# Kernel tuning notes

Measured on AMD Instinct MI355X. Metric: run time of the kernel, lower is better.

Reference implementation:

```python
import jax, jax.numpy as jnp
import numpy as np

PIXEL_THRESHOLD = 0.4
FRACTION_THRESHOLD = 0.03
NUM_CLASSES = 20
N, H, W = 100, 640, 960
LOGIT_SCALE = 8.0  # makes the instance-axis softmax peaky enough to cross PIXEL_THRESHOLD


def setup_inputs() -> dict:
    key = jax.random.key(0)
    k1, k2, k3 = jax.random.split(key, 3)
    cls_prob = jax.random.uniform(k1, (N,), dtype=jnp.float32)
    mask_prob = jax.random.normal(k2, (N, H, W), dtype=jnp.float32) * LOGIT_SCALE
    cls_idx = jax.random.randint(k3, (N,), 0, NUM_CLASSES)
    return {"cls_prob": cls_prob, "mask_prob": mask_prob, "cls_idx": cls_idx}


def _mask_removal(cls_prob, mask_prob, cls_idx):
    # Sort instances by class confidence, descending (greedy NMS order).
    order = jnp.argsort(-cls_prob)
    cls_prob_s = cls_prob[order]          # [N]
    cls_idx_s = cls_idx[order]            # [N]
    raw_s = mask_prob[order]              # [N,H,W] pre-softmax logits (mask_prob_copy)
    # Per-pixel softmax over the instance axis (permutation-equivariant, so
    # softmax-then-sort == sort-then-softmax as in the original).
    sm = jax.nn.softmax(raw_s, axis=0)    # [N,H,W]

    def step(state, inp):
        panoptic, mask_image = state      # [H,W], [C,H,W]
        smi, rawi, ci = inp
        logit = (smi >= PIXEL_THRESHOLD).astype(rawi.dtype)   # binarized mask [H,W]
        mask_sum = logit.sum()
        curr = mask_image[ci]
        overlap = jnp.sum((curr >= 1.0) & (logit == 1.0)).astype(rawi.dtype) / jnp.maximum(mask_sum, 1.0)
        degenerate = (logit.max() == logit.min()) | (mask_sum == 0.0)
        skip = degenerate | (overlap > FRACTION_THRESHOLD)
        # assign only unclaimed panoptic pixels inside the binarized mask
        assign = (panoptic == 0.0) & (logit == 1.0) & jnp.logical_not(skip)
        keep_mask = jnp.where(assign, rawi, 0.0)              # use_mask_low_constant=False
        panoptic = jnp.where(assign, 1.0, panoptic)
        mask_image = mask_image.at[ci].add(jnp.where(assign, logit, 0.0))
        return (panoptic, mask_image), (keep_mask, jnp.logical_not(skip))

    init = (jnp.zeros((H, W), jnp.float32), jnp.zeros((NUM_CLASSES, H, W), jnp.float32))
    _, (keep_masks, keep_flags) = jax.lax.scan(step, init, (sm, raw_s, cls_idx_s))
    # Fixed-shape outputs: keep_flags marks which (sorted) instances survived;
    # dropped instances have all-zero keep_masks rows.
    return cls_prob_s, keep_masks, cls_idx_s, keep_flags


def reference(cls_prob, mask_prob, cls_idx):
    return _mask_removal(cls_prob, mask_prob, cls_idx)
```

## Files before the change

### kernel.cpp

```cpp
#include <hip/hip_runtime.h>
#include <cstdint>
#include <cstddef>

#define N_INST 100
#define HW (640 * 960)
#define PIX_THR 0.4f
#define FRAC_THR 0.03f

#define OUT_MASKS_OFF 100
#define OUT_CLSIDX_OFF (100 + (size_t)N_INST * HW)
#define OUT_FLAGS_OFF (100 + (size_t)N_INST * HW + N_INST)


__global__ void k0_sort(const float* __restrict__ cls_prob,
                        const int* __restrict__ cls_idx,
                        int* __restrict__ ord,
                        float* __restrict__ out) {
    int i = threadIdx.x;
    if (i >= N_INST) return;
    float pi = cls_prob[i];
    int rank = 0;
    for (int j = 0; j < N_INST; ++j) {
        float pj = cls_prob[j];
        rank += (pj > pi) || (pj == pi && j < i);
    }
    ord[rank] = i;
    out[rank] = pi;
    out[OUT_CLSIDX_OFF + rank] = (float)cls_idx[i];
}

__global__ __launch_bounds__(256) void k1_softmax(
    const float* __restrict__ mask,
    const int* __restrict__ ord,
    unsigned* __restrict__ mask_sum,
    unsigned* __restrict__ pair_cnt,
    unsigned* __restrict__ code) {
    __shared__ int sord[N_INST];
    __shared__ unsigned ssum[N_INST];
    int t = threadIdx.x;
    if (t < N_INST) {
        sord[t] = ord[t];
        ssum[t] = 0u;
    }
    __syncthreads();

    int p = blockIdx.x * 256 + t;

    float v[N_INST];
#pragma unroll
    for (int i = 0; i < N_INST; ++i)
        v[i] = mask[(size_t)sord[i] * HW + p];

    float m = v[0];
    int p1 = 0;
    float m2 = -3.4e38f;
    int p2 = 0;
#pragma unroll
    for (int i = 1; i < N_INST; ++i) {
        if (v[i] > m) { m2 = m; p2 = p1; m = v[i]; p1 = i; }
        else if (v[i] > m2) { m2 = v[i]; p2 = i; }
    }

    float d = 0.0f;
#pragma unroll
    for (int i = 0; i < N_INST; ++i)
        d += expf(v[i] - m);

    float sm1 = 1.0f / d;
    float sm2 = expf(m2 - m) / d;
    bool q1 = (sm1 >= PIX_THR);
    bool q2 = (sm2 >= PIX_THR);

    unsigned c = 0u;
    if (q1) {
        atomicAdd(&ssum[p1], 1u);
        if (q2) {
            atomicAdd(&ssum[p2], 1u);
            int a = min(p1, p2);
            int b = max(p1, p2);
            atomicAdd(&pair_cnt[a * N_INST + b], 1u);
            c = (unsigned)(a + 1) | ((unsigned)(b + 1) << 8);
        } else {
            c = (unsigned)(p1 + 1);
        }
    }
    code[p] = c;

    __syncthreads();
    if (t < N_INST && ssum[t] != 0u)
        atomicAdd(&mask_sum[t], ssum[t]);
}

__global__ void k2_scan(const unsigned* __restrict__ mask_sum,
                        const unsigned* __restrict__ pair_cnt,
                        const int* __restrict__ ord,
                        const int* __restrict__ cls_idx,
                        int* __restrict__ keep,
                        float* __restrict__ out) {
    __shared__ unsigned spair[N_INST * N_INST];
    __shared__ int scls[N_INST];
    __shared__ unsigned sms[N_INST];
    __shared__ int skeep[N_INST];
    int t = threadIdx.x;
    for (int i = t; i < N_INST * N_INST; i += 256)
        spair[i] = pair_cnt[i];
    if (t < N_INST) {
        scls[t] = cls_idx[ord[t]];
        sms[t] = mask_sum[t];
    }
    __syncthreads();

    for (int b = 0; b < N_INST; ++b) {
        if (t < 64) {
            unsigned cnt = 0u;
            for (int a = t; a < b; a += 64)
                if (skeep[a] && scls[a] == scls[b])
                    cnt += spair[a * N_INST + b];
#pragma unroll
            for (int off = 32; off; off >>= 1)
                cnt += __shfl_down((int)cnt, off);
            if (t == 0) {
                unsigned ms = sms[b];
                float overlap = (float)cnt / fmaxf((float)ms, 1.0f);
                bool degen = (ms == 0u) || (ms == (unsigned)HW);
                bool skip = degen || (overlap > FRAC_THR);
                skeep[b] = skip ? 0 : 1;
            }
        }
        __syncthreads();
    }

    if (t < N_INST) {
        keep[t] = skeep[t];
        out[OUT_FLAGS_OFF + t] = (float)skeep[t];
    }
}

__global__ __launch_bounds__(256) void k3_write(
    const float* __restrict__ mask,
    const int* __restrict__ ord,
    const int* __restrict__ keep,
    const unsigned* __restrict__ code,
    float* __restrict__ out) {
    __shared__ int skeep[N_INST];
    __shared__ int sord[N_INST];
    if (threadIdx.x < N_INST) {
        skeep[threadIdx.x] = keep[threadIdx.x];
        sord[threadIdx.x] = ord[threadIdx.x];
    }
    __syncthreads();

    int i = blockIdx.y;
    int p = blockIdx.x * 256 + threadIdx.x;

    unsigned c = code[p];
    int a = (int)(c & 0xFFu) - 1;
    int b = (int)(c >> 8) - 1;

    bool assigned;
    if (a == i)      assigned = (skeep[i] != 0);
    else if (b == i) assigned = (skeep[i] != 0) && (skeep[a] == 0);
    else             assigned = false;

    float val = 0.0f;
    if (assigned)
        val = mask[(size_t)sord[i] * HW + p];
    out[OUT_MASKS_OFF + (size_t)i * HW + p] = val;
}

extern "C" void kernel_launch(void* const* d_in, const int* in_sizes, int n_in,
                              void* d_out, int out_size, void* d_ws, size_t ws_size,
                              hipStream_t stream) {
    const float* cls_prob = (const float*)d_in[0];
    const float* mask = (const float*)d_in[1];
    const int* cls_idx = (const int*)d_in[2];
    float* out = (float*)d_out;

    char* ws = (char*)d_ws;
    int* ord = (int*)(ws + 0);
    int* keep = (int*)(ws + 512);
    unsigned* mask_sum = (unsigned*)(ws + 1024);
    unsigned* pair_cnt = (unsigned*)(ws + 2048);
    unsigned* code = (unsigned*)(ws + 65536);

    hipMemsetAsync(ws + 1024, 0, 1024 + 40000, stream);

    k0_sort<<<1, 128, 0, stream>>>(cls_prob, cls_idx, ord, out);
    k1_softmax<<<HW / 256, 256, 0, stream>>>(mask, ord, mask_sum, pair_cnt, code);
    k2_scan<<<1, 256, 0, stream>>>(mask_sum, pair_cnt, ord, cls_idx, keep, out);
    k3_write<<<dim3(HW / 256, N_INST), 256, 0, stream>>>(mask, ord, keep, code, out);
}
```

Baseline: 288.9 us.

## Use online softmax with float4 loads, border repair pass, and one-read mask writer

Result: slower. 335.7 us (+16.2%).

```diff
diff --git a/kernel.cpp b/kernel.cpp
--- a/kernel.cpp
+++ b/kernel.cpp
@@ -6,6 +6,8 @@
 #define HW (640 * 960)
 #define PIX_THR 0.4f
 #define FRAC_THR 0.03f
+#define EPS_BORDER 5e-5f
+#define FLAG_CAP 65536
 
 #define OUT_MASKS_OFF 100
 #define OUT_CLSIDX_OFF (100 + (size_t)N_INST * HW)
@@ -29,66 +31,145 @@
     out[OUT_CLSIDX_OFF + rank] = (float)cls_idx[i];
 }
 
-__global__ __launch_bounds__(256) void k1_softmax(
+__global__ __launch_bounds__(256) void k1_online(
     const float* __restrict__ mask,
     const int* __restrict__ ord,
     unsigned* __restrict__ mask_sum,
     unsigned* __restrict__ pair_cnt,
-    unsigned* __restrict__ code) {
-    __shared__ int sord[N_INST];
+    unsigned* __restrict__ code,
+    unsigned* __restrict__ flag_count,
+    unsigned* __restrict__ flag_list) {
+    __shared__ size_t srow[N_INST];
     __shared__ unsigned ssum[N_INST];
     int t = threadIdx.x;
     if (t < N_INST) {
-        sord[t] = ord[t];
+        srow[t] = (size_t)ord[t] * HW;
         ssum[t] = 0u;
     }
     __syncthreads();
 
-    int p = blockIdx.x * 256 + t;
-
-    float v[N_INST];
-#pragma unroll
-    for (int i = 0; i < N_INST; ++i)
-        v[i] = mask[(size_t)sord[i] * HW + p];
-
-    float m = v[0];
-    int p1 = 0;
-    float m2 = -3.4e38f;
-    int p2 = 0;
-#pragma unroll
+    int p0 = (blockIdx.x * 256 + t) * 4;
+
+    float m[4], m2[4], d[4];
+    int i1[4], i2[4];
+    {
+        const float4 v4 = *(const float4*)(mask + srow[0] + p0);
+        const float vv[4] = {v4.x, v4.y, v4.z, v4.w};
+#pragma unroll
+        for (int j = 0; j < 4; ++j) {
+            m[j] = vv[j];
+            m2[j] = -3.4e38f;
+            d[j] = 1.0f;
+            i1[j] = 0;
+            i2[j] = 0;
+        }
+    }
+
+#pragma unroll 2
     for (int i = 1; i < N_INST; ++i) {
-        if (v[i] > m) { m2 = m; p2 = p1; m = v[i]; p1 = i; }
-        else if (v[i] > m2) { m2 = v[i]; p2 = i; }
-    }
-
-    float d = 0.0f;
-#pragma unroll
-    for (int i = 0; i < N_INST; ++i)
-        d += expf(v[i] - m);
-
-    float sm1 = 1.0f / d;
-    float sm2 = expf(m2 - m) / d;
-    bool q1 = (sm1 >= PIX_THR);
-    bool q2 = (sm2 >= PIX_THR);
-
-    unsigned c = 0u;
-    if (q1) {
-        atomicAdd(&ssum[p1], 1u);
-        if (q2) {
-            atomicAdd(&ssum[p2], 1u);
-            int a = min(p1, p2);
-            int b = max(p1, p2);
-            atomicAdd(&pair_cnt[a * N_INST + b], 1u);
-            c = (unsigned)(a + 1) | ((unsigned)(b + 1) << 8);
-        } else {
-            c = (unsigned)(p1 + 1);
-        }
-    }
-    code[p] = c;
+        const float4 v4 = *(const float4*)(mask + srow[i] + p0);
+        const float vv[4] = {v4.x, v4.y, v4.z, v4.w};
+#pragma unroll
+        for (int j = 0; j < 4; ++j) {
+            float v = vv[j];
+            float om = m[j], om2 = m2[j];
+            bool gt = v > om;
+            float nm = gt ? v : om;
+            d[j] = d[j] * expf(om - nm) + expf(v - nm);
+            m2[j] = gt ? om : (v > om2 ? v : om2);
+            i2[j] = gt ? i1[j] : (v > om2 ? i : i2[j]);
+            i1[j] = gt ? i : i1[j];
+            m[j] = nm;
+        }
+    }
+
+    unsigned c4[4];
+#pragma unroll
+    for (int j = 0; j < 4; ++j) {
+        float sm1 = 1.0f / d[j];
+        float sm2 = expf(m2[j] - m[j]) / d[j];
+        bool q1 = sm1 >= PIX_THR;
+        bool border = (fabsf(sm1 - PIX_THR) < EPS_BORDER) ||
+                      (q1 && fabsf(sm2 - PIX_THR) < EPS_BORDER);
+        unsigned c = 0u;
+        if (border) {
+            unsigned slot = atomicAdd(flag_count, 1u);
+            if (slot < FLAG_CAP) flag_list[slot] = (unsigned)(p0 + j);
+        } else if (q1) {
+            bool q2 = sm2 >= PIX_THR;
+            int a = i1[j], b = i2[j];
+            atomicAdd(&ssum[a], 1u);
+            if (q2) {
+                atomicAdd(&ssum[b], 1u);
+                int lo = min(a, b), hi = max(a, b);
+                atomicAdd(&pair_cnt[lo * N_INST + hi], 1u);
+                c = (unsigned)(lo + 1) | ((unsigned)(hi + 1) << 8);
+            } else {
+                c = (unsigned)(a + 1);
+            }
+        }
+        c4[j] = c;
+    }
+    *(uint4*)(code + p0) = make_uint4(c4[0], c4[1], c4[2], c4[3]);
 
     __syncthreads();
     if (t < N_INST && ssum[t] != 0u)
         atomicAdd(&mask_sum[t], ssum[t]);
+}
+
+__global__ void k1_repair(const float* __restrict__ mask,
+                          const int* __restrict__ ord,
+                          unsigned* __restrict__ mask_sum,
+                          unsigned* __restrict__ pair_cnt,
+                          unsigned* __restrict__ code,
+                          const unsigned* __restrict__ flag_count,
+                          const unsigned* __restrict__ flag_list) {
+    __shared__ int sord[N_INST];
+    if (threadIdx.x < N_INST) sord[threadIdx.x] = ord[threadIdx.x];
+    __syncthreads();
+
+    unsigned n = *flag_count;
+    if (n > FLAG_CAP) n = FLAG_CAP;
+    for (unsigned idx = blockIdx.x * blockDim.x + threadIdx.x; idx < n;
+         idx += gridDim.x * blockDim.x) {
+        int p = (int)flag_list[idx];
+        float v[N_INST];
+#pragma unroll
+        for (int i = 0; i < N_INST; ++i)
+            v[i] = mask[(size_t)sord[i] * HW + p];
+
+        float m = v[0];
+        int p1 = 0;
+        float m2 = -3.4e38f;
+        int p2 = 0;
+#pragma unroll
+        for (int i = 1; i < N_INST; ++i) {
+            if (v[i] > m) { m2 = m; p2 = p1; m = v[i]; p1 = i; }
+            else if (v[i] > m2) { m2 = v[i]; p2 = i; }
+        }
+        float d = 0.0f;
+#pragma unroll
+        for (int i = 0; i < N_INST; ++i)
+            d += expf(v[i] - m);
+
+        float sm1 = 1.0f / d;
+        float sm2 = expf(m2 - m) / d;
+        bool q1 = (sm1 >= PIX_THR);
+        bool q2 = (sm2 >= PIX_THR);
+        unsigned c = 0u;
+        if (q1) {
+            atomicAdd(&mask_sum[p1], 1u);
+            if (q2) {
+                atomicAdd(&mask_sum[p2], 1u);
+                int lo = min(p1, p2), hi = max(p1, p2);
+                atomicAdd(&pair_cnt[lo * N_INST + hi], 1u);
+                c = (unsigned)(lo + 1) | ((unsigned)(hi + 1) << 8);
+            } else {
+                c = (unsigned)(p1 + 1);
+            }
+        }
+        code[p] = c;
+    }
 }
 
 __global__ void k2_scan(const unsigned* __restrict__ mask_sum,
@@ -144,28 +225,43 @@
     float* __restrict__ out) {
     __shared__ int skeep[N_INST];
     __shared__ int sord[N_INST];
-    if (threadIdx.x < N_INST) {
-        skeep[threadIdx.x] = keep[threadIdx.x];
-        sord[threadIdx.x] = ord[threadIdx.x];
-    }
-    __syncthreads();
-
-    int i = blockIdx.y;
-    int p = blockIdx.x * 256 + threadIdx.x;
-
-    unsigned c = code[p];
-    int a = (int)(c & 0xFFu) - 1;
-    int b = (int)(c >> 8) - 1;
-
-    bool assigned;
-    if (a == i)      assigned = (skeep[i] != 0);
-    else if (b == i) assigned = (skeep[i] != 0) && (skeep[a] == 0);
-    else             assigned = false;
-
-    float val = 0.0f;
-    if (assigned)
-        val = mask[(size_t)sord[i] * HW + p];
-    out[OUT_MASKS_OFF + (size_t)i * HW + p] = val;
+    int t = threadIdx.x;
+    if (t < N_INST) {
+        skeep[t] = keep[t];
+        sord[t] = ord[t];
+    }
+    __syncthreads();
+
+    int p0 = (blockIdx.x * 256 + t) * 4;
+    uint4 c4 = *(const uint4*)(code + p0);
+    unsigned cc[4] = {c4.x, c4.y, c4.z, c4.w};
+
+    int inst[4];
+    float val[4];
+#pragma unroll
+    for (int j = 0; j < 4; ++j) {
+        unsigned c = cc[j];
+        int a = (int)(c & 0xFFu) - 1;
+        int b = (int)(c >> 8) - 1;
+        int as = -1;
+        if (a >= 0) {
+            if (skeep[a]) as = a;
+            else if (b >= 0 && skeep[b]) as = b;
+        }
+        inst[j] = as;
+        val[j] = (as >= 0) ? mask[(size_t)sord[as] * HW + p0 + j] : 0.0f;
+    }
+
+    int i0 = blockIdx.y * (N_INST / 4);
+    int i1 = i0 + (N_INST / 4);
+    for (int i = i0; i < i1; ++i) {
+        float4 o;
+        o.x = (inst[0] == i) ? val[0] : 0.0f;
+        o.y = (inst[1] == i) ? val[1] : 0.0f;
+        o.z = (inst[2] == i) ? val[2] : 0.0f;
+        o.w = (inst[3] == i) ? val[3] : 0.0f;
+        *(float4*)(out + OUT_MASKS_OFF + (size_t)i * HW + p0) = o;
+    }
 }
 
 extern "C" void kernel_launch(void* const* d_in, const int* in_sizes, int n_in,
@@ -180,13 +276,18 @@
     int* ord = (int*)(ws + 0);
     int* keep = (int*)(ws + 512);
     unsigned* mask_sum = (unsigned*)(ws + 1024);
+    unsigned* flag_count = (unsigned*)(ws + 1536);
     unsigned* pair_cnt = (unsigned*)(ws + 2048);
     unsigned* code = (unsigned*)(ws + 65536);
+    unsigned* flag_list = (unsigned*)(ws + 2523136);
 
     hipMemsetAsync(ws + 1024, 0, 1024 + 40000, stream);
 
     k0_sort<<<1, 128, 0, stream>>>(cls_prob, cls_idx, ord, out);
-    k1_softmax<<<HW / 256, 256, 0, stream>>>(mask, ord, mask_sum, pair_cnt, code);
+    k1_online<<<HW / 1024, 256, 0, stream>>>(mask, ord, mask_sum, pair_cnt,
+                                             code, flag_count, flag_list);
+    k1_repair<<<16, 256, 0, stream>>>(mask, ord, mask_sum, pair_cnt, code,
+                                      flag_count, flag_list);
     k2_scan<<<1, 256, 0, stream>>>(mask_sum, pair_cnt, ord, cls_idx, keep, out);
-    k3_write<<<dim3(HW / 256, N_INST), 256, 0, stream>>>(mask, ord, keep, code, out);
-}
+    k3_write<<<dim3(HW / 1024, 4), 256, 0, stream>>>(mask, ord, keep, code, out);
+}
```

## Stream softmax in natural order, cache kept logits, scatter into memset output

Applied to the files above, without the earlier changes.

Result: faster. 235.6 us (-18.5%).

```diff
diff --git a/kernel.cpp b/kernel.cpp
--- a/kernel.cpp
+++ b/kernel.cpp
@@ -6,89 +6,183 @@
 #define HW (640 * 960)
 #define PIX_THR 0.4f
 #define FRAC_THR 0.03f
+#define EPS_BORDER 5e-5f
+#define FLAG_CAP 65536
+#define L2E 1.4426950408889634f
 
 #define OUT_MASKS_OFF 100
 #define OUT_CLSIDX_OFF (100 + (size_t)N_INST * HW)
 #define OUT_FLAGS_OFF (100 + (size_t)N_INST * HW + N_INST)
 
 
-__global__ void k0_sort(const float* __restrict__ cls_prob,
-                        const int* __restrict__ cls_idx,
-                        int* __restrict__ ord,
-                        float* __restrict__ out) {
-    int i = threadIdx.x;
-    if (i >= N_INST) return;
-    float pi = cls_prob[i];
-    int rank = 0;
-    for (int j = 0; j < N_INST; ++j) {
-        float pj = cls_prob[j];
-        rank += (pj > pi) || (pj == pi && j < i);
-    }
-    ord[rank] = i;
-    out[rank] = pi;
-    out[OUT_CLSIDX_OFF + rank] = (float)cls_idx[i];
-}
-
-__global__ __launch_bounds__(256) void k1_softmax(
+__global__ __launch_bounds__(256) void k0_init(
+    const float* __restrict__ cls_prob,
+    const int* __restrict__ cls_idx,
+    int* __restrict__ ord,
+    int* __restrict__ rank_arr,
+    float* __restrict__ out,
+    unsigned* __restrict__ mask_sum,
+    unsigned* __restrict__ flag_count,
+    unsigned* __restrict__ pair_cnt) {
+    int t = threadIdx.x;
+    if (t < N_INST) {
+        float pi = cls_prob[t];
+        int rank = 0;
+        for (int j = 0; j < N_INST; ++j) {
+            float pj = cls_prob[j];
+            rank += (pj > pi) || (pj == pi && j < t);
+        }
+        ord[rank] = t;
+        rank_arr[t] = rank;
+        out[rank] = pi;
+        out[OUT_CLSIDX_OFF + rank] = (float)cls_idx[t];
+        mask_sum[t] = 0u;
+    }
+    if (t == 0) *flag_count = 0u;
+    for (int i = t; i < N_INST * N_INST; i += 256)
+        pair_cnt[i] = 0u;
+}
+
+__global__ __launch_bounds__(256) void k1_main(
     const float* __restrict__ mask,
-    const int* __restrict__ ord,
+    const int* __restrict__ rank_arr,
     unsigned* __restrict__ mask_sum,
     unsigned* __restrict__ pair_cnt,
-    unsigned* __restrict__ code) {
-    __shared__ int sord[N_INST];
+    uint4* __restrict__ pvals,
+    unsigned* __restrict__ flag_count,
+    unsigned* __restrict__ flag_list) {
+    __shared__ int srank[N_INST];
     __shared__ unsigned ssum[N_INST];
     int t = threadIdx.x;
     if (t < N_INST) {
-        sord[t] = ord[t];
+        srank[t] = rank_arr[t];
         ssum[t] = 0u;
     }
     __syncthreads();
 
-    int p = blockIdx.x * 256 + t;
-
-    float v[N_INST];
-#pragma unroll
-    for (int i = 0; i < N_INST; ++i)
-        v[i] = mask[(size_t)sord[i] * HW + p];
-
-    float m = v[0];
-    int p1 = 0;
-    float m2 = -3.4e38f;
-    int p2 = 0;
-#pragma unroll
-    for (int i = 1; i < N_INST; ++i) {
-        if (v[i] > m) { m2 = m; p2 = p1; m = v[i]; p1 = i; }
-        else if (v[i] > m2) { m2 = v[i]; p2 = i; }
-    }
-
-    float d = 0.0f;
-#pragma unroll
-    for (int i = 0; i < N_INST; ++i)
-        d += expf(v[i] - m);
-
-    float sm1 = 1.0f / d;
-    float sm2 = expf(m2 - m) / d;
-    bool q1 = (sm1 >= PIX_THR);
-    bool q2 = (sm2 >= PIX_THR);
-
-    unsigned c = 0u;
-    if (q1) {
-        atomicAdd(&ssum[p1], 1u);
-        if (q2) {
-            atomicAdd(&ssum[p2], 1u);
-            int a = min(p1, p2);
-            int b = max(p1, p2);
-            atomicAdd(&pair_cnt[a * N_INST + b], 1u);
-            c = (unsigned)(a + 1) | ((unsigned)(b + 1) << 8);
-        } else {
-            c = (unsigned)(p1 + 1);
-        }
-    }
-    code[p] = c;
+    int p0 = (blockIdx.x * 256 + t) * 2;
+    const float* base = mask + p0;
+
+    float S[2] = {0.0f, 0.0f};
+    float m[2] = {-3.4e38f, -3.4e38f};
+    float n[2] = {-3.4e38f, -3.4e38f};
+    int ia[2] = {0, 0};
+    int ib[2] = {0, 0};
+
+#pragma unroll 10
+    for (int i = 0; i < N_INST; ++i) {
+        float2 v2 = *(const float2*)(base + (size_t)i * HW);
+        float vv[2] = {v2.x, v2.y};
+#pragma unroll
+        for (int j = 0; j < 2; ++j) {
+            float v = vv[j];
+            S[j] += exp2f(v * L2E);
+            bool gt = v > m[j];
+            bool g2 = v > n[j];
+            n[j] = fmaxf(n[j], fminf(m[j], v));
+            ib[j] = gt ? ia[j] : (g2 ? i : ib[j]);
+            ia[j] = gt ? i : ia[j];
+            m[j] = fmaxf(m[j], v);
+        }
+    }
+
+#pragma unroll
+    for (int j = 0; j < 2; ++j) {
+        int p = p0 + j;
+        float e1 = exp2f(m[j] * L2E);
+        float e2 = exp2f(n[j] * L2E);
+        float t04 = 0.4f * S[j];
+        float w = EPS_BORDER * S[j];
+        bool q1 = e1 >= t04;
+        bool border = (fabsf(e1 - t04) < w) || (q1 && fabsf(e2 - t04) < w);
+
+        unsigned c = 0u;
+        float vlo = 0.0f, vhi = 0.0f;
+        if (border) {
+            unsigned slot = atomicAdd(flag_count, 1u);
+            if (slot < FLAG_CAP) flag_list[slot] = (unsigned)p;
+        } else if (q1) {
+            bool q2 = e2 >= t04;
+            int r1 = srank[ia[j]];
+            atomicAdd(&ssum[r1], 1u);
+            if (q2) {
+                int r2 = srank[ib[j]];
+                atomicAdd(&ssum[r2], 1u);
+                int lo = min(r1, r2), hi = max(r1, r2);
+                atomicAdd(&pair_cnt[lo * N_INST + hi], 1u);
+                c = (unsigned)(lo + 1) | ((unsigned)(hi + 1) << 8);
+                vlo = (r1 < r2) ? m[j] : n[j];
+                vhi = (r1 < r2) ? n[j] : m[j];
+            } else {
+                c = (unsigned)(r1 + 1);
+                vlo = m[j];
+            }
+        }
+        pvals[p] = make_uint4(c, __float_as_uint(vlo), __float_as_uint(vhi), 0u);
+    }
 
     __syncthreads();
     if (t < N_INST && ssum[t] != 0u)
         atomicAdd(&mask_sum[t], ssum[t]);
+}
+
+__global__ void k1_repair(const float* __restrict__ mask,
+                          const int* __restrict__ ord,
+                          unsigned* __restrict__ mask_sum,
+                          unsigned* __restrict__ pair_cnt,
+                          uint4* __restrict__ pvals,
+                          const unsigned* __restrict__ flag_count,
+                          const unsigned* __restrict__ flag_list) {
+    __shared__ int sord[N_INST];
+    if (threadIdx.x < N_INST) sord[threadIdx.x] = ord[threadIdx.x];
+    __syncthreads();
+
+    unsigned nf = *flag_count;
+    if (nf > FLAG_CAP) nf = FLAG_CAP;
+    for (unsigned idx = blockIdx.x * blockDim.x + threadIdx.x; idx < nf;
+         idx += gridDim.x * blockDim.x) {
+        int p = (int)flag_list[idx];
+        float v[N_INST];
+#pragma unroll
+        for (int i = 0; i < N_INST; ++i)
+            v[i] = mask[(size_t)sord[i] * HW + p];
+
+        float m = v[0];
+        int p1 = 0;
+        float m2 = -3.4e38f;
+        int p2 = 0;
+#pragma unroll
+        for (int i = 1; i < N_INST; ++i) {
+            if (v[i] > m) { m2 = m; p2 = p1; m = v[i]; p1 = i; }
+            else if (v[i] > m2) { m2 = v[i]; p2 = i; }
+        }
+        float d = 0.0f;
+#pragma unroll
+        for (int i = 0; i < N_INST; ++i)
+            d += expf(v[i] - m);
+
+        float sm1 = 1.0f / d;
+        float sm2 = expf(m2 - m) / d;
+        bool q1 = (sm1 >= PIX_THR);
+        bool q2 = (sm2 >= PIX_THR);
+        unsigned c = 0u;
+        float vlo = 0.0f, vhi = 0.0f;
+        if (q1) {
+            atomicAdd(&mask_sum[p1], 1u);
+            if (q2) {
+                atomicAdd(&mask_sum[p2], 1u);
+                int lo = min(p1, p2), hi = max(p1, p2);
+                atomicAdd(&pair_cnt[lo * N_INST + hi], 1u);
+                c = (unsigned)(lo + 1) | ((unsigned)(hi + 1) << 8);
+                vlo = v[lo];
+                vhi = v[hi];
+            } else {
+                c = (unsigned)(p1 + 1);
+                vlo = v[p1];
+            }
+        }
+        pvals[p] = make_uint4(c, __float_as_uint(vlo), __float_as_uint(vhi), 0u);
+    }
 }
 
 __global__ void k2_scan(const unsigned* __restrict__ mask_sum,
@@ -136,36 +230,33 @@
     }
 }
 
-__global__ __launch_bounds__(256) void k3_write(
-    const float* __restrict__ mask,
-    const int* __restrict__ ord,
+__global__ __launch_bounds__(256) void k3_scatter(
+    const uint4* __restrict__ pvals,
     const int* __restrict__ keep,
-    const unsigned* __restrict__ code,
     float* __restrict__ out) {
     __shared__ int skeep[N_INST];
-    __shared__ int sord[N_INST];
-    if (threadIdx.x < N_INST) {
-        skeep[threadIdx.x] = keep[threadIdx.x];
-        sord[threadIdx.x] = ord[threadIdx.x];
-    }
-    __syncthreads();
-
-    int i = blockIdx.y;
+    if (threadIdx.x < N_INST) skeep[threadIdx.x] = keep[threadIdx.x];
+    __syncthreads();
+
     int p = blockIdx.x * 256 + threadIdx.x;
-
-    unsigned c = code[p];
+    uint4 pv = pvals[p];
+    unsigned c = pv.x;
+    if (c == 0u) return;
     int a = (int)(c & 0xFFu) - 1;
     int b = (int)(c >> 8) - 1;
 
-    bool assigned;
-    if (a == i)      assigned = (skeep[i] != 0);
-    else if (b == i) assigned = (skeep[i] != 0) && (skeep[a] == 0);
-    else             assigned = false;
-
-    float val = 0.0f;
-    if (assigned)
-        val = mask[(size_t)sord[i] * HW + p];
-    out[OUT_MASKS_OFF + (size_t)i * HW + p] = val;
+    int inst;
+    float val;
+    if (skeep[a]) {
+        inst = a;
+        val = __uint_as_float(pv.y);
+    } else if (b >= 0 && skeep[b]) {
+        inst = b;
+        val = __uint_as_float(pv.z);
+    } else {
+        return;
+    }
+    out[OUT_MASKS_OFF + (size_t)inst * HW + p] = val;
 }
 
 extern "C" void kernel_launch(void* const* d_in, const int* in_sizes, int n_in,
@@ -178,15 +269,22 @@
 
     char* ws = (char*)d_ws;
     int* ord = (int*)(ws + 0);
-    int* keep = (int*)(ws + 512);
-    unsigned* mask_sum = (unsigned*)(ws + 1024);
-    unsigned* pair_cnt = (unsigned*)(ws + 2048);
-    unsigned* code = (unsigned*)(ws + 65536);
-
-    hipMemsetAsync(ws + 1024, 0, 1024 + 40000, stream);
-
-    k0_sort<<<1, 128, 0, stream>>>(cls_prob, cls_idx, ord, out);
-    k1_softmax<<<HW / 256, 256, 0, stream>>>(mask, ord, mask_sum, pair_cnt, code);
+    int* rank_arr = (int*)(ws + 512);
+    int* keep = (int*)(ws + 1024);
+    unsigned* mask_sum = (unsigned*)(ws + 1536);
+    unsigned* flag_count = (unsigned*)(ws + 2048);
+    unsigned* pair_cnt = (unsigned*)(ws + 4096);
+    uint4* pvals = (uint4*)(ws + 65536);
+    unsigned* flag_list = (unsigned*)(ws + 65536 + (size_t)HW * 16);
+
+    hipMemsetAsync(d_out, 0, (size_t)out_size * sizeof(float), stream);
+
+    k0_init<<<1, 256, 0, stream>>>(cls_prob, cls_idx, ord, rank_arr, out,
+                                   mask_sum, flag_count, pair_cnt);
+    k1_main<<<HW / 512, 256, 0, stream>>>(mask, rank_arr, mask_sum, pair_cnt,
+                                          pvals, flag_count, flag_list);
+    k1_repair<<<16, 256, 0, stream>>>(mask, ord, mask_sum, pair_cnt, pvals,
+                                      flag_count, flag_list);
     k2_scan<<<1, 256, 0, stream>>>(mask_sum, pair_cnt, ord, cls_idx, keep, out);
-    k3_write<<<dim3(HW / 256, N_INST), 256, 0, stream>>>(mask, ord, keep, code, out);
-}
+    k3_scatter<<<HW / 256, 256, 0, stream>>>(pvals, keep, out);
+}
```
